# Optimization experiments

Hardware: AMD Instinct MI355X
Metric: run time of the kernel (lower is better)

The kernel has to match this reference:

```python
import jax, jax.numpy as jnp
import numpy as np

N = 500_000        # batch rows
K_OLD = 128        # old bins -> 129 edges
K_NEW = 100        # new bins -> 101 edges


def setup_inputs() -> dict:
    key = jax.random.key(0)
    logits = jax.random.normal(key, (N, K_OLD), dtype=jnp.float32)
    # strictly increasing edge grids (monotone, mismatched resolution)
    old_edges = jnp.linspace(0.0, 1.0, K_OLD + 1, dtype=jnp.float32)
    new_edges = jnp.linspace(0.0, 1.0, K_NEW + 1, dtype=jnp.float32)
    return {"logits": logits, "old_edges": old_edges, "new_edges": new_edges}


def reference(logits, old_edges, new_edges):
    # softmax over bins -> per-bin probability mass
    probs = jax.nn.softmax(logits, axis=-1)                      # [N, K_old]
    widths = old_edges[1:] - old_edges[:-1]                      # [K_old]
    density = probs / widths                                     # [N, K_old]
    # overlap[i, j] = length of intersection of old bin i with new bin j.
    # Equivalent to the per-new-bin mask/gather/sum loop in _rebin_pc:
    # bins with no strict overlap contribute exactly 0 after the clip.
    overlap = jnp.clip(
        jnp.minimum(old_edges[1:, None], new_edges[None, 1:])
        - jnp.maximum(old_edges[:-1, None], new_edges[None, :-1]),
        0.0,
    )                                                            # [K_old, K_new]
    rebinned = density @ overlap                                 # [N, K_new]
    eps = jnp.finfo(rebinned.dtype).tiny
    return jnp.log(rebinned + eps)
```

## Files before the change

### kernel.cpp

```cpp
#include <hip/hip_runtime.h>
#include <math.h>

#define KOLD 128
#define KNEW 100
#define GPB  8

typedef float f32x4 __attribute__((ext_vector_type(4)));

#define FT_OFF  1024
#define ROW_B   416
#define WAVE_B  (4 * ROW_B)
#define LDS_BYTES (FT_OFF + 4 * WAVE_B)

template <int CTRL, int ROWM>
__device__ __forceinline__ float dpp_add(float v) {
    int s = __builtin_amdgcn_update_dpp(0, __float_as_int(v), CTRL, ROWM, 0xf, true);
    return v + __int_as_float(s);
}
__device__ __forceinline__ float scan32(float v) {
    v = dpp_add<0x111, 0xf>(v);
    v = dpp_add<0x112, 0xf>(v);
    v = dpp_add<0x114, 0xf>(v);
    v = dpp_add<0x118, 0xf>(v);
    v = dpp_add<0x142, 0xa>(v);
    return v;
}
__device__ __forceinline__ float grp_total(float scanned, int half) {
    int t0 = __builtin_amdgcn_readlane(__float_as_int(scanned), 31);
    int t1 = __builtin_amdgcn_readlane(__float_as_int(scanned), 63);
    return __int_as_float(half ? t1 : t0);
}

__launch_bounds__(256, 8)
__global__ void rebin_k(const float* __restrict__ logits,
                        const float* __restrict__ oe,
                        const float* __restrict__ ne,
                        float* __restrict__ out, int nrows)
{
    __shared__ __align__(16) char lds[LDS_BYTES];
    int*   tmp_i = (int*)(lds + 0);
    float* tmp_t = (float*)(lds + 512);

    const int tid  = threadIdx.x;
    const int lane = tid & 63;
    const int wid  = tid >> 6;
    const int c    = lane & 31;
    const int half = lane >> 5;

    if (tid <= KNEW) {
        float e = ne[tid];
        int i = 0;
#pragma unroll
        for (int st = 64; st >= 1; st >>= 1) {
            int cand = i + st;
            if (cand <= KOLD - 1 && oe[cand] <= e) i = cand;
        }
        float a = oe[i], b = oe[i + 1];
        float tt = (e - a) / (b - a);
        tmp_i[tid] = i;
        tmp_t[tid] = fminf(fmaxf(tt, 0.f), 1.f);
    }
    __syncthreads();

    int k0 = 0;
#pragma unroll
    for (int st = 64; st >= 1; st >>= 1) {
        int cand = k0 + st;
        if (cand <= KNEW + 1 && tmp_i[cand - 1] < 4 * c) k0 = cand;
    }
    unsigned kb[4];
    float    te[4];
    int      se[4];
#pragma unroll
    for (int e = 0; e < 4; ++e) {
        int k  = k0 + e;
        int kc = k <= KNEW ? k : KNEW;
        int ib = tmp_i[kc];
        bool ok = (k <= KNEW) && (ib < 4 * c + 4);
        kb[e] = ok ? (unsigned)(k * 4) : 102u * 4u;
        te[e] = ok ? tmp_t[kc] : 0.f;
        se[e] = ok ? (ib - 4 * c) : 0;
    }

    char* fW = lds + FT_OFF + wid * WAVE_B;
    const int nm1 = nrows - 1;
    const int ngroups = (nrows + 15) >> 4;
    const int gmax = ngroups - 1;
    const float tiny = 1.1754943508222875e-38f;
    const int grp0 = blockIdx.x * GPB;

    float4 vA, vB;
    {
        const int g  = grp0 <= gmax ? grp0 : gmax;
        const int w0 = g * 16 + wid * 4;
        const size_t offA = (size_t)min(w0 + half, nm1) * KOLD + c * 4;
        const size_t offB = (size_t)min(w0 + 2 + half, nm1) * KOLD + c * 4;
        vA = *(const float4*)(logits + offA);
        vB = *(const float4*)(logits + offB);
    }

#pragma unroll 1
    for (int kg = 0; kg < GPB; ++kg) {
        const int grp = grp0 + kg;
        if (grp >= ngroups) break;
        const int wrow0 = grp * 16 + wid * 4;

        float4 nA, nB;
        {
            const int gn = (grp + 1) <= gmax ? (grp + 1) : gmax;
            const int wn = gn * 16 + wid * 4;
            const size_t offA = (size_t)min(wn + half, nm1) * KOLD + c * 4;
            const size_t offB = (size_t)min(wn + 2 + half, nm1) * KOLD + c * 4;
            nA = *(const float4*)(logits + offA);
            nB = *(const float4*)(logits + offB);
        }

        {
            const float e0 = __expf(fminf(fmaxf(vA.x, -80.f), 80.f));
            const float e1 = __expf(fminf(fmaxf(vA.y, -80.f), 80.f));
            const float e2 = __expf(fminf(fmaxf(vA.z, -80.f), 80.f));
            const float e3 = __expf(fminf(fmaxf(vA.w, -80.f), 80.f));
            const float sl = (e0 + e1) + (e2 + e3);
            const float ic = scan32(sl);
            const float tot = grp_total(ic, half);
            float rc = __builtin_amdgcn_rcpf(tot);
            const float inv = rc * (2.0f - tot * rc);
            const float p0 = ic - sl;
            const float p1 = p0 + e0, p2 = p1 + e1, p3 = p2 + e2;
            char* frow = fW + half * ROW_B;
#pragma unroll
            for (int e = 0; e < 4; ++e) {
                const float f0 = fmaf(te[e], e0, p0);
                const float f1 = fmaf(te[e], e1, p1);
                const float f2 = fmaf(te[e], e2, p2);
                const float f3 = fmaf(te[e], e3, p3);
                const float g01 = (se[e] & 1) ? f1 : f0;
                const float g23 = (se[e] & 1) ? f3 : f2;
                const float F   = (se[e] & 2) ? g23 : g01;
                *(float*)(frow + kb[e]) = F * inv;
            }
        }
        {
            const float e0 = __expf(fminf(fmaxf(vB.x, -80.f), 80.f));
            const float e1 = __expf(fminf(fmaxf(vB.y, -80.f), 80.f));
            const float e2 = __expf(fminf(fmaxf(vB.z, -80.f), 80.f));
            const float e3 = __expf(fminf(fmaxf(vB.w, -80.f), 80.f));
            const float sl = (e0 + e1) + (e2 + e3);
            const float ic = scan32(sl);
            const float tot = grp_total(ic, half);
            float rc = __builtin_amdgcn_rcpf(tot);
            const float inv = rc * (2.0f - tot * rc);
            const float p0 = ic - sl;
            const float p1 = p0 + e0, p2 = p1 + e1, p3 = p2 + e2;
            char* frow = fW + (2 + half) * ROW_B;
#pragma unroll
            for (int e = 0; e < 4; ++e) {
                const float f0 = fmaf(te[e], e0, p0);
                const float f1 = fmaf(te[e], e1, p1);
                const float f2 = fmaf(te[e], e2, p2);
                const float f3 = fmaf(te[e], e3, p3);
                const float g01 = (se[e] & 1) ? f1 : f0;
                const float g23 = (se[e] & 1) ? f3 : f2;
                const float F   = (se[e] & 2) ? g23 : g01;
                *(float*)(frow + kb[e]) = F * inv;
            }
        }
        asm volatile("s_waitcnt lgkmcnt(0)" ::: "memory");

        float* gout = out + (size_t)wrow0 * KNEW;
#pragma unroll
        for (int it = 0; it < 2; ++it) {
            const int t  = it * 64 + lane;
            const int tc = t < 100 ? t : 99;
            const int r  = (tc * 41) >> 10;
            const int q  = tc - r * 25;
            const char* frow = fW + r * ROW_B + q * 16;
            const float4 F4 = *(const float4*)(frow);
            const float  F5 = *(const float*)(frow + 16);
            f32x4 o;
            o.x = __logf(fmaxf(F4.y - F4.x, 0.f) + tiny);
            o.y = __logf(fmaxf(F4.z - F4.y, 0.f) + tiny);
            o.z = __logf(fmaxf(F4.w - F4.z, 0.f) + tiny);
            o.w = __logf(fmaxf(F5  - F4.w, 0.f) + tiny);
            if (t < 100 && wrow0 + r < nrows) {
                __builtin_nontemporal_store(o, (f32x4*)(gout + r * KNEW + q * 4));
            }
        }
        asm volatile("" ::: "memory");

        vA = nA; vB = nB;
    }
}

extern "C" void kernel_launch(void* const* d_in, const int* in_sizes, int n_in,
                              void* d_out, int out_size, void* d_ws, size_t ws_size,
                              hipStream_t stream) {
    const float* logits = (const float*)d_in[0];
    const float* oe     = (const float*)d_in[1];
    const float* ne     = (const float*)d_in[2];
    float* out          = (float*)d_out;
    const int nrows     = in_sizes[0] / KOLD;

    const int ngroups = (nrows + 15) / 16;
    const int blocks  = (ngroups + GPB - 1) / GPB;
    rebin_k<<<blocks, 256, 0, stream>>>(logits, oe, ne, out, nrows);
}
```

Before: 83.18 us.

## Deepen logits prefetch to two groups ahead and pad LDS row stride

The register prefetch of input logits now runs two row-groups ahead instead of one, with an extra pair of float4 buffers rotated each iteration, to hide more global-memory latency. The LDS row stride goes from 416 to 420 bytes, and the readback switches from a float4 plus a scalar to five scalar loads, since rows are no longer 16-byte aligned. The padding is meant to cut LDS bank conflicts across rows, but it costs more LDS load instructions and more registers, which could lower occupancy.

```diff
diff --git a/kernel.cpp b/kernel.cpp
--- a/kernel.cpp
+++ b/kernel.cpp
@@ -8,7 +8,7 @@
 typedef float f32x4 __attribute__((ext_vector_type(4)));
 
 #define FT_OFF  1024
-#define ROW_B   416
+#define ROW_B   420
 #define WAVE_B  (4 * ROW_B)
 #define LDS_BYTES (FT_OFF + 4 * WAVE_B)
 
@@ -89,14 +89,16 @@
     const float tiny = 1.1754943508222875e-38f;
     const int grp0 = blockIdx.x * GPB;
 
-    float4 vA, vB;
+    float4 vA, vB, wA, wB;
     {
-        const int g  = grp0 <= gmax ? grp0 : gmax;
-        const int w0 = g * 16 + wid * 4;
-        const size_t offA = (size_t)min(w0 + half, nm1) * KOLD + c * 4;
-        const size_t offB = (size_t)min(w0 + 2 + half, nm1) * KOLD + c * 4;
-        vA = *(const float4*)(logits + offA);
-        vB = *(const float4*)(logits + offB);
+        const int g0 = grp0 <= gmax ? grp0 : gmax;
+        const int w0 = g0 * 16 + wid * 4;
+        vA = *(const float4*)(logits + (size_t)min(w0 + half, nm1) * KOLD + c * 4);
+        vB = *(const float4*)(logits + (size_t)min(w0 + 2 + half, nm1) * KOLD + c * 4);
+        const int g1 = (grp0 + 1) <= gmax ? (grp0 + 1) : gmax;
+        const int w1 = g1 * 16 + wid * 4;
+        wA = *(const float4*)(logits + (size_t)min(w1 + half, nm1) * KOLD + c * 4);
+        wB = *(const float4*)(logits + (size_t)min(w1 + 2 + half, nm1) * KOLD + c * 4);
     }
 
 #pragma unroll 1
@@ -107,12 +109,10 @@
 
         float4 nA, nB;
         {
-            const int gn = (grp + 1) <= gmax ? (grp + 1) : gmax;
+            const int gn = (grp + 2) <= gmax ? (grp + 2) : gmax;
             const int wn = gn * 16 + wid * 4;
-            const size_t offA = (size_t)min(wn + half, nm1) * KOLD + c * 4;
-            const size_t offB = (size_t)min(wn + 2 + half, nm1) * KOLD + c * 4;
-            nA = *(const float4*)(logits + offA);
-            nB = *(const float4*)(logits + offB);
+            nA = *(const float4*)(logits + (size_t)min(wn + half, nm1) * KOLD + c * 4);
+            nB = *(const float4*)(logits + (size_t)min(wn + 2 + half, nm1) * KOLD + c * 4);
         }
 
         {
@@ -174,21 +174,24 @@
             const int tc = t < 100 ? t : 99;
             const int r  = (tc * 41) >> 10;
             const int q  = tc - r * 25;
-            const char* frow = fW + r * ROW_B + q * 16;
-            const float4 F4 = *(const float4*)(frow);
-            const float  F5 = *(const float*)(frow + 16);
+            const float* fp = (const float*)(fW + r * ROW_B) + q * 4;
+            const float F0 = fp[0];
+            const float F1 = fp[1];
+            const float F2 = fp[2];
+            const float F3 = fp[3];
+            const float F4 = fp[4];
             f32x4 o;
-            o.x = __logf(fmaxf(F4.y - F4.x, 0.f) + tiny);
-            o.y = __logf(fmaxf(F4.z - F4.y, 0.f) + tiny);
-            o.z = __logf(fmaxf(F4.w - F4.z, 0.f) + tiny);
-            o.w = __logf(fmaxf(F5  - F4.w, 0.f) + tiny);
+            o.x = __logf(fmaxf(F1 - F0, 0.f) + tiny);
+            o.y = __logf(fmaxf(F2 - F1, 0.f) + tiny);
+            o.z = __logf(fmaxf(F3 - F2, 0.f) + tiny);
+            o.w = __logf(fmaxf(F4 - F3, 0.f) + tiny);
             if (t < 100 && wrow0 + r < nrows) {
                 __builtin_nontemporal_store(o, (f32x4*)(gout + r * KNEW + q * 4));
             }
         }
         asm volatile("" ::: "memory");
 
-        vA = nA; vB = nB;
+        vA = wA; vB = wB; wA = nA; wB = nB;
     }
 }
 
```

Result: slower. 87.47 us (+5.2%).
